# Kernel optimization log

Measured on AMD Instinct MI355X. Metric: run time of the kernel, lower is better.

Reference implementation:

```python
import jax, jax.numpy as jnp
import numpy as np

N_NODES = 100000
N_EDGES = 1600000
N_GRAPHS = 512
F_IN = 128
HID = 128
N_CLS = 10


def setup_inputs() -> dict:
    key = jax.random.key(0)
    ks = jax.random.split(key, 12)
    x = jax.random.normal(ks[0], (N_NODES, F_IN), dtype=jnp.float32)
    edge_index = jax.random.randint(ks[1], (2, N_EDGES), 0, N_NODES, dtype=jnp.int64)
    batch = jnp.sort(jax.random.randint(ks[2], (N_NODES,), 0, N_GRAPHS, dtype=jnp.int64))
    def glorot(k, shape):
        lim = float(np.sqrt(6.0 / (shape[0] + shape[1])))
        return jax.random.uniform(k, shape, jnp.float32, -lim, lim)
    return {
        "x": x, "edge_index": edge_index, "batch": batch,
        "W1": glorot(ks[3], (F_IN, HID)), "b1": jnp.zeros((HID,), jnp.float32),
        "W2": glorot(ks[4], (HID, HID)), "b2": jnp.zeros((HID,), jnp.float32),
        "W3": glorot(ks[5], (HID, HID)), "b3": jnp.zeros((HID,), jnp.float32),
        "Wc1": glorot(ks[6], (2 * HID, HID)), "bc1": jnp.zeros((HID,), jnp.float32),
        "Wc2": glorot(ks[7], (HID, N_CLS)), "bc2": jnp.zeros((N_CLS,), jnp.float32),
    }


def _gcn_layer(h, W, b, src, dst, dinv_sqrt, norm):
    # GCNConv: transform, then symmetric-normalized aggregation with self-loops.
    h = h @ W                                    # [N, HID]
    msgs = h[src] * norm[:, None]                # gather + scale  [E, HID]
    agg = jax.ops.segment_sum(msgs, dst, num_segments=N_NODES)
    agg = agg + h * (dinv_sqrt * dinv_sqrt)[:, None]   # self-loop term (1/deg)
    return jax.nn.relu(agg + b)


def reference(x, edge_index, batch, W1, b1, W2, b2, W3, b3, Wc1, bc1, Wc2, bc2):
    src, dst = edge_index[0], edge_index[1]
    # degree including self loop (counted at aggregation target = dst)
    deg = jax.ops.segment_sum(jnp.ones((N_EDGES,), jnp.float32), dst,
                              num_segments=N_NODES) + 1.0
    dinv_sqrt = jax.lax.rsqrt(deg)
    norm = dinv_sqrt[src] * dinv_sqrt[dst]       # [E]

    h = _gcn_layer(x, W1, b1, src, dst, dinv_sqrt, norm)
    h = _gcn_layer(h, W2, b2, src, dst, dinv_sqrt, norm)
    h = _gcn_layer(h, W3, b3, src, dst, dinv_sqrt, norm)

    # mean_max pooling over graphs
    counts = jax.ops.segment_sum(jnp.ones((N_NODES,), jnp.float32), batch,
                                 num_segments=N_GRAPHS)
    sums = jax.ops.segment_sum(h, batch, num_segments=N_GRAPHS)
    g_mean = sums / jnp.maximum(counts, 1.0)[:, None]
    g_max = jax.ops.segment_max(h, batch, num_segments=N_GRAPHS)
    g_max = jnp.where(counts[:, None] > 0, g_max, 0.0)
    g = jnp.concatenate([g_mean, g_max], axis=1)  # [G, 2*HID]

    # MLP head (dropout is identity in eval mode)
    hcls = jax.nn.relu(g @ Wc1 + bc1)
    return hcls @ Wc2 + bc2                       # [G, N_CLS]
```

## Files before the change

kernel.cpp:

```cpp
#include <hip/hip_runtime.h>
#include <hip/hip_bf16.h>
#include <hip/hip_fp16.h>

#define HIDDIM 128
#define NABLK 256
#define EPB 6250
#define BCAP 5120

typedef __attribute__((ext_vector_type(8))) _Float16 half8;
typedef __attribute__((ext_vector_type(4))) float f32x4;

__device__ __forceinline__ int scan256_incl(int v, int* sbuf, int t) {
    sbuf[t] = v;
    __syncthreads();
    for (int off = 1; off < 256; off <<= 1) {
        int x = sbuf[t];
        if (t >= off) x += sbuf[t - off];
        __syncthreads();
        sbuf[t] = x;
        __syncthreads();
    }
    return sbuf[t];
}

__global__ __launch_bounds__(1024) void k_bucketA(const int* __restrict__ ei, int E,
                                                  int2* __restrict__ sortedA,
                                                  int* __restrict__ tableA, int nbuck) {
    __shared__ int2 sEdge[EPB];
    __shared__ int hist[512];
    __shared__ int sb[512];
    int t = threadIdx.x;
    int blk = blockIdx.x;
    int base = blk * EPB;
    int cnt = min(EPB, E - base);
    if (t < 512) hist[t] = 0;
    __syncthreads();
    int es[7], ed[7], rk[7];
#pragma unroll
    for (int it = 0; it < 7; ++it) {
        int i = it * 1024 + t;
        es[it] = 0; ed[it] = -1; rk[it] = 0;
        if (i < cnt) {
            es[it] = ei[base + i];
            ed[it] = ei[E + base + i];
            rk[it] = atomicAdd(&hist[ed[it] >> 8], 1);
        }
    }
    __syncthreads();
    if (t < 512) sb[t] = hist[t];
    __syncthreads();
    for (int off = 1; off < 512; off <<= 1) {
        int x = 0;
        if (t < 512) { x = sb[t]; if (t >= off) x += sb[t - off]; }
        __syncthreads();
        if (t < 512) sb[t] = x;
        __syncthreads();
    }
#pragma unroll
    for (int it = 0; it < 7; ++it) {
        if (ed[it] >= 0) {
            int b = ed[it] >> 8;
            int slot = sb[b] - hist[b] + rk[it];
            sEdge[slot] = make_int2(es[it], ed[it]);
        }
    }
    if (t <= nbuck) tableA[t * NABLK + blk] = sb[t] - hist[t];
    __syncthreads();
    for (int j = t; j < cnt; j += 1024) sortedA[base + j] = sEdge[j];
}

__global__ void k_btot(const int* __restrict__ tableA, int* __restrict__ tot) {
    __shared__ int red[4];
    int b = blockIdx.x;
    int t = threadIdx.x;
    int v = tableA[(b + 1) * NABLK + t] - tableA[b * NABLK + t];
    for (int off = 32; off; off >>= 1) v += __shfl_down(v, off, 64);
    if ((t & 63) == 0) red[t >> 6] = v;
    __syncthreads();
    if (t == 0) tot[b] = red[0] + red[1] + red[2] + red[3];
}

__global__ void k_bbase(const int* __restrict__ tot, int* __restrict__ bbase, int nbuck) {
    __shared__ int sb[512];
    int t = threadIdx.x;
    int v = (t < nbuck) ? tot[t] : 0;
    sb[t] = v;
    __syncthreads();
    for (int off = 1; off < 512; off <<= 1) {
        int x = sb[t];
        if (t >= off) x += sb[t - off];
        __syncthreads();
        sb[t] = x;
        __syncthreads();
    }
    if (t < nbuck) bbase[t] = sb[t] - v;
}

__global__ __launch_bounds__(256) void k_bucketB(const int2* __restrict__ sortedA,
                                                 const int* __restrict__ tableA,
                                                 const int* __restrict__ bbase,
                                                 int* __restrict__ csr_src,
                                                 int* __restrict__ row_off,
                                                 float* __restrict__ dinv, int N) {
    __shared__ int2 eIn[BCAP];
    __shared__ int h[256];
    __shared__ int cur[256];
    __shared__ int scanbuf[256];
    int b = blockIdx.x;
    int t = threadIdx.x;
    int s = tableA[b * NABLK + t];
    int c = tableA[(b + 1) * NABLK + t] - s;
    int rIncl = scan256_incl(c, scanbuf, t);
    int rOff = rIncl - c;
    int nE = scanbuf[255];
    for (int k = 0; k < c; ++k) {
        int p = rOff + k;
        if (p < BCAP) eIn[p] = sortedA[t * EPB + s + k];
    }
    h[t] = 0;
    __syncthreads();
    if (nE > BCAP) nE = BCAP;
    for (int j = t; j < nE; j += 256) atomicAdd(&h[eIn[j].y & 255], 1);
    __syncthreads();
    int deg = h[t];
    int nIncl = scan256_incl(deg, scanbuf, t);
    int nOff = nIncl - deg;
    int g = b * 256 + t;
    int bb = bbase[b];
    if (g < N) {
        dinv[g] = rsqrtf((float)deg + 1.0f);
        row_off[g + 1] = bb + nIncl;
        if (g == 0) row_off[0] = 0;
    }
    cur[t] = nOff;
    __syncthreads();
    for (int j = t; j < nE; j += 256) {
        int2 e = eIn[j];
        int sl = atomicAdd(&cur[e.y & 255], 1);
        csr_src[bb + sl] = e.x;
    }
}

__global__ __launch_bounds__(256) void k_wprep(const float* __restrict__ W1,
                                               const float* __restrict__ W2,
                                               const float* __restrict__ W3,
                                               __half* __restrict__ Whf,
                                               __half* __restrict__ Wdf) {
    int layer = blockIdx.x;
    const float* W = layer == 0 ? W1 : (layer == 1 ? W2 : W3);
    __half* oh = Whf + (size_t)layer * 16384;
    __half* od = Wdf + (size_t)layer * 16384;
    int t = threadIdx.x;
#pragma unroll
    for (int i = 0; i < 8; ++i) {
        int fr = t * 8 + i;
        int kk = fr >> 9;
        int jt = (fr >> 6) & 7;
        int lane = fr & 63;
        int col = jt * 16 + (lane & 15);
        int kbase = kk * 32 + ((lane >> 4) << 3);
        __half hv[8], dv[8];
#pragma unroll
        for (int e = 0; e < 8; ++e) {
            float v = W[(kbase + e) * 128 + col];
            __half h = __float2half_rn(v);
            hv[e] = h;
            dv[e] = __float2half_rn(v - __half2float(h));
        }
        *(uint4*)(oh + (size_t)fr * 8) = *(uint4*)hv;
        *(uint4*)(od + (size_t)fr * 8) = *(uint4*)dv;
    }
}

__global__ __launch_bounds__(256) void k_gemm(const float* __restrict__ A,
                                              const __half* __restrict__ Bh,
                                              const __half* __restrict__ Bd,
                                              __half* __restrict__ Oh, int nrows) {
    int wave = threadIdx.x >> 6, lane = threadIdx.x & 63;
    int row0 = blockIdx.x * 64 + wave * 16;
    int arow = row0 + (lane & 15);
    if (arow >= nrows) arow = nrows - 1;
    int kg = lane >> 4;
    const float* ap = A + (size_t)arow * 128 + kg * 8;
    f32x4 acc[8];
#pragma unroll
    for (int j = 0; j < 8; ++j) acc[j] = (f32x4){0.f, 0.f, 0.f, 0.f};

#pragma unroll
    for (int kk = 0; kk < 4; ++kk) {
        float4 a0 = *(const float4*)(ap + kk * 32);
        float4 a1 = *(const float4*)(ap + kk * 32 + 4);
        float av[8] = {a0.x, a0.y, a0.z, a0.w, a1.x, a1.y, a1.z, a1.w};
        half8 ah, da;
#pragma unroll
        for (int e = 0; e < 8; ++e) {
            _Float16 h = (_Float16)av[e];
            ah[e] = h;
            da[e] = (_Float16)(av[e] - (float)h);
        }
        const half8* bhp = (const half8*)(Bh + ((size_t)(kk * 8) * 64 + lane) * 8);
        const half8* bdp = (const half8*)(Bd + ((size_t)(kk * 8) * 64 + lane) * 8);
#pragma unroll
        for (int jt = 0; jt < 8; ++jt) {
            half8 bh = bhp[jt * 64];
            half8 bd = bdp[jt * 64];
            acc[jt] = __builtin_amdgcn_mfma_f32_16x16x32_f16(ah, bh, acc[jt], 0, 0, 0);
            acc[jt] = __builtin_amdgcn_mfma_f32_16x16x32_f16(da, bh, acc[jt], 0, 0, 0);
            acc[jt] = __builtin_amdgcn_mfma_f32_16x16x32_f16(ah, bd, acc[jt], 0, 0, 0);
        }
    }
    int ocol = lane & 15;
    int orow_base = row0 + (lane >> 4) * 4;
#pragma unroll
    for (int r = 0; r < 4; ++r) {
        int orow = orow_base + r;
        if (orow < nrows) {
#pragma unroll
            for (int jt = 0; jt < 8; ++jt)
                Oh[(size_t)orow * 128 + jt * 16 + ocol] = __float2half_rn(acc[jt][r]);
        }
    }
}

__global__ __launch_bounds__(256) void k_agg(const __half* __restrict__ hH,
                                             const int* __restrict__ row_off,
                                             const int* __restrict__ csr_src,
                                             const float* __restrict__ dinv,
                                             const float* __restrict__ bias,
                                             float* __restrict__ out, int n) {
    int node = blockIdx.x * 4 + (threadIdx.x >> 6);
    int lane = threadIdx.x & 63;
    if (node >= n) return;
    int half = lane >> 5;
    int q = lane & 31;
    float dd = dinv[node];
    int s = row_off[node], e = row_off[node + 1];
    int cnt = e - s;
    const int* __restrict__ cp = csr_src + s;
    float4 acc = make_float4(0.f, 0.f, 0.f, 0.f);
    for (int t = 0; t < cnt; t += 8) {
        int idx[4];
        float nm[4];
#pragma unroll
        for (int p = 0; p < 4; ++p) {
            int tt = t + 2 * p + half;
            bool ok = tt < cnt;
            idx[p] = cp[ok ? tt : 0];
            nm[p] = ok ? dd : 0.f;
        }
        float dsv[4];
#pragma unroll
        for (int p = 0; p < 4; ++p) dsv[p] = dinv[idx[p]];
        uint2 w[4];
#pragma unroll
        for (int p = 0; p < 4; ++p)
            w[p] = *(const uint2*)((const char*)hH + (((size_t)(unsigned)idx[p]) << 8) + ((unsigned)q << 3));
#pragma unroll
        for (int p = 0; p < 4; ++p) {
            float norm = nm[p] * dsv[p];
            float2 f0 = __half22float2(*(const __half2*)&w[p].x);
            float2 f1 = __half22float2(*(const __half2*)&w[p].y);
            acc.x = fmaf(norm, f0.x, acc.x);
            acc.y = fmaf(norm, f0.y, acc.y);
            acc.z = fmaf(norm, f1.x, acc.z);
            acc.w = fmaf(norm, f1.y, acc.w);
        }
    }
    acc.x += __shfl_xor(acc.x, 32);
    acc.y += __shfl_xor(acc.y, 32);
    acc.z += __shfl_xor(acc.z, 32);
    acc.w += __shfl_xor(acc.w, 32);
    if (half == 0) {
        float d2 = dd * dd;
        uint2 sw = *(const uint2*)((const char*)hH + ((size_t)(unsigned)node << 8) + ((unsigned)q << 3));
        float2 s0 = __half22float2(*(const __half2*)&sw.x);
        float2 s1 = __half22float2(*(const __half2*)&sw.y);
        float4 bb = *(const float4*)(bias + q * 4);
        float4 o;
        o.x = fmaxf(fmaf(d2, s0.x, acc.x) + bb.x, 0.f);
        o.y = fmaxf(fmaf(d2, s0.y, acc.y) + bb.y, 0.f);
        o.z = fmaxf(fmaf(d2, s1.x, acc.z) + bb.z, 0.f);
        o.w = fmaxf(fmaf(d2, s1.y, acc.w) + bb.w, 0.f);
        *(float4*)(out + (size_t)node * 128 + q * 4) = o;
    }
}

__global__ void k_pool(const float* __restrict__ h, const int* __restrict__ batch,
                       float* __restrict__ gsum, float* __restrict__ gmax,
                       int* __restrict__ gcnt, int n) {
    int t = threadIdx.x;
    int start = blockIdx.x * 64;
    if (start >= n) return;
    int end = min(start + 64, n);
    int cur = batch[start];
    float s = 0.f, m = 0.f;
    int c = 0;
    for (int i = start; i < end; ++i) {
        int g = batch[i];
        if (g != cur) {
            atomicAdd(&gsum[cur * 128 + t], s);
            atomicMax((int*)&gmax[cur * 128 + t], __float_as_int(m));
            if (t == 0) atomicAdd(&gcnt[cur], c);
            s = 0.f; m = 0.f; c = 0; cur = g;
        }
        float v = h[(size_t)i * 128 + t];
        s += v;
        m = fmaxf(m, v);
        c++;
    }
    atomicAdd(&gsum[cur * 128 + t], s);
    atomicMax((int*)&gmax[cur * 128 + t], __float_as_int(m));
    if (t == 0) atomicAdd(&gcnt[cur], c);
}

__global__ void k_head(const float* __restrict__ gsum, const float* __restrict__ gmax,
                       const int* __restrict__ gcnt, const float* __restrict__ Wc1,
                       const float* __restrict__ bc1, const float* __restrict__ Wc2,
                       const float* __restrict__ bc2, float* __restrict__ out, int G) {
    __shared__ float gv[256];
    __shared__ float hc[128];
    int g = blockIdx.x;
    if (g >= G) return;
    int t = threadIdx.x;
    float c = (float)gcnt[g];
    float inv = 1.0f / fmaxf(c, 1.0f);
    gv[t] = gsum[g * 128 + t] * inv;
    gv[128 + t] = gmax[g * 128 + t];
    __syncthreads();
    float a = bc1[t];
#pragma unroll 8
    for (int k = 0; k < 256; ++k) a = fmaf(gv[k], Wc1[k * 128 + t], a);
    hc[t] = fmaxf(a, 0.f);
    __syncthreads();
    if (t < 10) {
        float o = bc2[t];
        for (int k = 0; k < 128; ++k) o = fmaf(hc[k], Wc2[k * 10 + t], o);
        out[g * 10 + t] = o;
    }
}

extern "C" void kernel_launch(void* const* d_in, const int* in_sizes, int n_in,
                              void* d_out, int out_size, void* d_ws, size_t ws_size,
                              hipStream_t stream) {
    const float* x   = (const float*)d_in[0];
    const int*   ei  = (const int*)d_in[1];
    const int*   bat = (const int*)d_in[2];
    const float* W1  = (const float*)d_in[3];
    const float* b1  = (const float*)d_in[4];
    const float* W2  = (const float*)d_in[5];
    const float* b2  = (const float*)d_in[6];
    const float* W3  = (const float*)d_in[7];
    const float* b3  = (const float*)d_in[8];
    const float* Wc1 = (const float*)d_in[9];
    const float* bc1 = (const float*)d_in[10];
    const float* Wc2 = (const float*)d_in[11];
    const float* bc2 = (const float*)d_in[12];
    float* out = (float*)d_out;

    const int N = in_sizes[0] / HIDDIM;
    const int E = in_sizes[1] / 2;
    const int G = out_size / 10;
    const int nbuck = (N + 255) >> 8;

    char* ws = (char*)d_ws;
    size_t off = 0;
    auto take = [&](size_t bytes) -> char* {
        char* p = ws + off;
        off += (bytes + 255) & ~(size_t)255;
        return p;
    };
    float* hA       = (float*)take((size_t)N * HIDDIM * 4);
    int2*  sortedA  = (int2*)hA;
    __half* hH      = (__half*)take((size_t)N * HIDDIM * 2);
    float* dinv     = (float*)take((size_t)N * 4);
    int*   row_off  = (int*)take(((size_t)N + 1) * 4);
    int*   tableA   = (int*)take((size_t)(nbuck + 1) * NABLK * 4);
    int*   tot      = (int*)take(512 * 4);
    int*   bbase    = (int*)take(512 * 4);
    int*   csr_src  = (int*)take((size_t)E * 4);
    float* gsum     = (float*)take((size_t)G * HIDDIM * 4);
    float* gmax     = (float*)take((size_t)G * HIDDIM * 4);
    int*   gcnt     = (int*)take((size_t)G * 4);
    __half* Whf     = (__half*)take((size_t)3 * 16384 * 2);
    __half* Wdf     = (__half*)take((size_t)3 * 16384 * 2);

    hipMemsetAsync(gsum, 0, (size_t)G * HIDDIM * 4, stream);
    hipMemsetAsync(gmax, 0, (size_t)G * HIDDIM * 4, stream);
    hipMemsetAsync(gcnt, 0, (size_t)G * 4, stream);

    k_bucketA<<<NABLK, 1024, 0, stream>>>(ei, E, sortedA, tableA, nbuck);
    k_btot<<<nbuck, 256, 0, stream>>>(tableA, tot);
    k_bbase<<<1, 512, 0, stream>>>(tot, bbase, nbuck);
    k_bucketB<<<nbuck, 256, 0, stream>>>(sortedA, tableA, bbase, csr_src, row_off, dinv, N);
    k_wprep<<<3, 256, 0, stream>>>(W1, W2, W3, Whf, Wdf);

    int gb = (N + 63) / 64;
    int ab = (N + 3) / 4;
    k_gemm<<<gb, 256, 0, stream>>>(x, Whf, Wdf, hH, N);
    k_agg<<<ab, 256, 0, stream>>>(hH, row_off, csr_src, dinv, b1, hA, N);
    k_gemm<<<gb, 256, 0, stream>>>(hA, Whf + 16384, Wdf + 16384, hH, N);
    k_agg<<<ab, 256, 0, stream>>>(hH, row_off, csr_src, dinv, b2, hA, N);
    k_gemm<<<gb, 256, 0, stream>>>(hA, Whf + 32768, Wdf + 32768, hH, N);
    k_agg<<<ab, 256, 0, stream>>>(hH, row_off, csr_src, dinv, b3, hA, N);

    k_pool<<<(N + 63) / 64, 128, 0, stream>>>(hA, bat, gsum, gmax, gcnt, N);
    k_head<<<G, 128, 0, stream>>>(gsum, gmax, gcnt, Wc1, bc1, Wc2, bc2, out, G);
}
```

Measured before the change: 369.3 us.

## Prescale GEMM output by dinv and store layer activations in fp16

The GEMM epilogue now multiplies each row by dinv[src], so aggregation becomes a plain sum of gathered rows followed by one dinv[dst] scale. This removes the per-edge dinv gather and multiply. Padded lanes point at a zeroed sentinel row instead of being masked. Activations between layers are stored in fp16 instead of fp32, which halves the write and read traffic for the GEMM and pool kernels, and a new fp16-input GEMM drops the A residual split, trading some precision for fewer MFMAs.

Measured after the change: 353.3 us. 1.05x faster.

```diff
diff --git a/kernel.cpp b/kernel.cpp
--- a/kernel.cpp
+++ b/kernel.cpp
@@ -172,10 +172,11 @@
     }
 }
 
-__global__ __launch_bounds__(256) void k_gemm(const float* __restrict__ A,
-                                              const __half* __restrict__ Bh,
-                                              const __half* __restrict__ Bd,
-                                              __half* __restrict__ Oh, int nrows) {
+__global__ __launch_bounds__(256) void k_gemm1(const float* __restrict__ A,
+                                               const __half* __restrict__ Bh,
+                                               const __half* __restrict__ Bd,
+                                               const float* __restrict__ dinv,
+                                               __half* __restrict__ Oh, int nrows) {
     int wave = threadIdx.x >> 6, lane = threadIdx.x & 63;
     int row0 = blockIdx.x * 64 + wave * 16;
     int arow = row0 + (lane & 15);
@@ -185,7 +186,6 @@
     f32x4 acc[8];
 #pragma unroll
     for (int j = 0; j < 8; ++j) acc[j] = (f32x4){0.f, 0.f, 0.f, 0.f};
-
 #pragma unroll
     for (int kk = 0; kk < 4; ++kk) {
         float4 a0 = *(const float4*)(ap + kk * 32);
@@ -215,19 +215,61 @@
     for (int r = 0; r < 4; ++r) {
         int orow = orow_base + r;
         if (orow < nrows) {
+            float dv = dinv[orow];
 #pragma unroll
             for (int jt = 0; jt < 8; ++jt)
-                Oh[(size_t)orow * 128 + jt * 16 + ocol] = __float2half_rn(acc[jt][r]);
-        }
-    }
-}
-
-__global__ __launch_bounds__(256) void k_agg(const __half* __restrict__ hH,
+                Oh[(size_t)orow * 128 + jt * 16 + ocol] = __float2half_rn(acc[jt][r] * dv);
+        }
+    }
+}
+
+__global__ __launch_bounds__(256) void k_gemm16(const __half* __restrict__ A,
+                                                const __half* __restrict__ Bh,
+                                                const __half* __restrict__ Bd,
+                                                const float* __restrict__ dinv,
+                                                __half* __restrict__ Oh, int nrows) {
+    int wave = threadIdx.x >> 6, lane = threadIdx.x & 63;
+    int row0 = blockIdx.x * 64 + wave * 16;
+    int arow = row0 + (lane & 15);
+    if (arow >= nrows) arow = nrows - 1;
+    int kg = lane >> 4;
+    const __half* ap = A + (size_t)arow * 128 + kg * 8;
+    f32x4 acc[8];
+#pragma unroll
+    for (int j = 0; j < 8; ++j) acc[j] = (f32x4){0.f, 0.f, 0.f, 0.f};
+#pragma unroll
+    for (int kk = 0; kk < 4; ++kk) {
+        half8 ah = *(const half8*)(ap + kk * 32);
+        const half8* bhp = (const half8*)(Bh + ((size_t)(kk * 8) * 64 + lane) * 8);
+        const half8* bdp = (const half8*)(Bd + ((size_t)(kk * 8) * 64 + lane) * 8);
+#pragma unroll
+        for (int jt = 0; jt < 8; ++jt) {
+            half8 bh = bhp[jt * 64];
+            half8 bd = bdp[jt * 64];
+            acc[jt] = __builtin_amdgcn_mfma_f32_16x16x32_f16(ah, bh, acc[jt], 0, 0, 0);
+            acc[jt] = __builtin_amdgcn_mfma_f32_16x16x32_f16(ah, bd, acc[jt], 0, 0, 0);
+        }
+    }
+    int ocol = lane & 15;
+    int orow_base = row0 + (lane >> 4) * 4;
+#pragma unroll
+    for (int r = 0; r < 4; ++r) {
+        int orow = orow_base + r;
+        if (orow < nrows) {
+            float dv = dinv[orow];
+#pragma unroll
+            for (int jt = 0; jt < 8; ++jt)
+                Oh[(size_t)orow * 128 + jt * 16 + ocol] = __float2half_rn(acc[jt][r] * dv);
+        }
+    }
+}
+
+__global__ __launch_bounds__(256) void k_agg(const __half* __restrict__ hHs,
                                              const int* __restrict__ row_off,
                                              const int* __restrict__ csr_src,
                                              const float* __restrict__ dinv,
                                              const float* __restrict__ bias,
-                                             float* __restrict__ out, int n) {
+                                             __half* __restrict__ outH, int n) {
     int node = blockIdx.x * 4 + (threadIdx.x >> 6);
     int lane = threadIdx.x & 63;
     if (node >= n) return;
@@ -240,30 +282,25 @@
     float4 acc = make_float4(0.f, 0.f, 0.f, 0.f);
     for (int t = 0; t < cnt; t += 8) {
         int idx[4];
-        float nm[4];
 #pragma unroll
         for (int p = 0; p < 4; ++p) {
             int tt = t + 2 * p + half;
             bool ok = tt < cnt;
-            idx[p] = cp[ok ? tt : 0];
-            nm[p] = ok ? dd : 0.f;
-        }
-        float dsv[4];
-#pragma unroll
-        for (int p = 0; p < 4; ++p) dsv[p] = dinv[idx[p]];
+            int raw = cp[ok ? tt : 0];
+            idx[p] = ok ? raw : n;
+        }
         uint2 w[4];
 #pragma unroll
         for (int p = 0; p < 4; ++p)
-            w[p] = *(const uint2*)((const char*)hH + (((size_t)(unsigned)idx[p]) << 8) + ((unsigned)q << 3));
+            w[p] = *(const uint2*)((const char*)hHs + (((size_t)(unsigned)idx[p]) << 8) + ((unsigned)q << 3));
 #pragma unroll
         for (int p = 0; p < 4; ++p) {
-            float norm = nm[p] * dsv[p];
             float2 f0 = __half22float2(*(const __half2*)&w[p].x);
             float2 f1 = __half22float2(*(const __half2*)&w[p].y);
-            acc.x = fmaf(norm, f0.x, acc.x);
-            acc.y = fmaf(norm, f0.y, acc.y);
-            acc.z = fmaf(norm, f1.x, acc.z);
-            acc.w = fmaf(norm, f1.y, acc.w);
+            acc.x += f0.x;
+            acc.y += f0.y;
+            acc.z += f1.x;
+            acc.w += f1.y;
         }
     }
     acc.x += __shfl_xor(acc.x, 32);
@@ -271,21 +308,20 @@
     acc.z += __shfl_xor(acc.z, 32);
     acc.w += __shfl_xor(acc.w, 32);
     if (half == 0) {
-        float d2 = dd * dd;
-        uint2 sw = *(const uint2*)((const char*)hH + ((size_t)(unsigned)node << 8) + ((unsigned)q << 3));
+        uint2 sw = *(const uint2*)((const char*)hHs + ((size_t)(unsigned)node << 8) + ((unsigned)q << 3));
         float2 s0 = __half22float2(*(const __half2*)&sw.x);
         float2 s1 = __half22float2(*(const __half2*)&sw.y);
         float4 bb = *(const float4*)(bias + q * 4);
-        float4 o;
-        o.x = fmaxf(fmaf(d2, s0.x, acc.x) + bb.x, 0.f);
-        o.y = fmaxf(fmaf(d2, s0.y, acc.y) + bb.y, 0.f);
-        o.z = fmaxf(fmaf(d2, s1.x, acc.z) + bb.z, 0.f);
-        o.w = fmaxf(fmaf(d2, s1.y, acc.w) + bb.w, 0.f);
-        *(float4*)(out + (size_t)node * 128 + q * 4) = o;
-    }
-}
-
-__global__ void k_pool(const float* __restrict__ h, const int* __restrict__ batch,
+        __half o[4];
+        o[0] = __float2half_rn(fmaxf(fmaf(dd, acc.x + s0.x, bb.x), 0.f));
+        o[1] = __float2half_rn(fmaxf(fmaf(dd, acc.y + s0.y, bb.y), 0.f));
+        o[2] = __float2half_rn(fmaxf(fmaf(dd, acc.z + s1.x, bb.z), 0.f));
+        o[3] = __float2half_rn(fmaxf(fmaf(dd, acc.w + s1.y, bb.w), 0.f));
+        *(uint2*)(outH + (size_t)node * 128 + q * 4) = *(uint2*)o;
+    }
+}
+
+__global__ void k_pool(const __half* __restrict__ h, const int* __restrict__ batch,
                        float* __restrict__ gsum, float* __restrict__ gmax,
                        int* __restrict__ gcnt, int n) {
     int t = threadIdx.x;
@@ -303,7 +339,7 @@
             if (t == 0) atomicAdd(&gcnt[cur], c);
             s = 0.f; m = 0.f; c = 0; cur = g;
         }
-        float v = h[(size_t)i * 128 + t];
+        float v = __half2float(h[(size_t)i * 128 + t]);
         s += v;
         m = fmaxf(m, v);
         c++;
@@ -369,9 +405,9 @@
         off += (bytes + 255) & ~(size_t)255;
         return p;
     };
-    float* hA       = (float*)take((size_t)N * HIDDIM * 4);
-    int2*  sortedA  = (int2*)hA;
-    __half* hH      = (__half*)take((size_t)N * HIDDIM * 2);
+    __half* aggH    = (__half*)take((size_t)N * HIDDIM * 2);
+    int2*  sortedA  = (int2*)aggH;
+    __half* hHs     = (__half*)take(((size_t)N + 1) * HIDDIM * 2);
     float* dinv     = (float*)take((size_t)N * 4);
     int*   row_off  = (int*)take(((size_t)N + 1) * 4);
     int*   tableA   = (int*)take((size_t)(nbuck + 1) * NABLK * 4);
@@ -387,6 +423,7 @@
     hipMemsetAsync(gsum, 0, (size_t)G * HIDDIM * 4, stream);
     hipMemsetAsync(gmax, 0, (size_t)G * HIDDIM * 4, stream);
     hipMemsetAsync(gcnt, 0, (size_t)G * 4, stream);
+    hipMemsetAsync(hHs + (size_t)N * HIDDIM, 0, HIDDIM * 2, stream);
 
     k_bucketA<<<NABLK, 1024, 0, stream>>>(ei, E, sortedA, tableA, nbuck);
     k_btot<<<nbuck, 256, 0, stream>>>(tableA, tot);
@@ -396,13 +433,13 @@
 
     int gb = (N + 63) / 64;
     int ab = (N + 3) / 4;
-    k_gemm<<<gb, 256, 0, stream>>>(x, Whf, Wdf, hH, N);
-    k_agg<<<ab, 256, 0, stream>>>(hH, row_off, csr_src, dinv, b1, hA, N);
-    k_gemm<<<gb, 256, 0, stream>>>(hA, Whf + 16384, Wdf + 16384, hH, N);
-    k_agg<<<ab, 256, 0, stream>>>(hH, row_off, csr_src, dinv, b2, hA, N);
-    k_gemm<<<gb, 256, 0, stream>>>(hA, Whf + 32768, Wdf + 32768, hH, N);
-    k_agg<<<ab, 256, 0, stream>>>(hH, row_off, csr_src, dinv, b3, hA, N);
-
-    k_pool<<<(N + 63) / 64, 128, 0, stream>>>(hA, bat, gsum, gmax, gcnt, N);
+    k_gemm1<<<gb, 256, 0, stream>>>(x, Whf, Wdf, dinv, hHs, N);
+    k_agg<<<ab, 256, 0, stream>>>(hHs, row_off, csr_src, dinv, b1, aggH, N);
+    k_gemm16<<<gb, 256, 0, stream>>>(aggH, Whf + 16384, Wdf + 16384, dinv, hHs, N);
+    k_agg<<<ab, 256, 0, stream>>>(hHs, row_off, csr_src, dinv, b2, aggH, N);
+    k_gemm16<<<gb, 256, 0, stream>>>(aggH, Whf + 32768, Wdf + 32768, dinv, hHs, N);
+    k_agg<<<ab, 256, 0, stream>>>(hHs, row_off, csr_src, dinv, b3, aggH, N);
+
+    k_pool<<<(N + 63) / 64, 128, 0, stream>>>(aggH, bat, gsum, gmax, gcnt, N);
     k_head<<<G, 128, 0, stream>>>(gsum, gmax, gcnt, Wc1, bc1, Wc2, bc2, out, G);
 }
```
